# Optimization experiments

Measured on AMD Instinct MI355X. Metric: run time of the kernel, lower is better.

## Reference

```python
import jax, jax.numpy as jnp
import numpy as np

POOLING_COUNTS = [15, 8, 8]
N = 128
D = 256
B = 16


def _build_specs():
    # Replicates the (kernel, stride, i, j) schedule of SparseConv.__init__.
    specs = []
    stride, offset = 1, 0
    for ci, c in enumerate(POOLING_COUNTS):
        for k in range(c):
            offset += stride
            i = np.arange(0, N - offset, stride)
            j = np.arange(offset, N, stride)
            kern = 3 if (ci > 0 and k == 0) else 2  # first conv of later groups downsamples
            st = 2 if (ci > 0 and k == 0) else 1
            specs.append((kern, st, i, j))
        stride *= 2
    return specs

SPECS = _build_specs()
N_K2 = sum(1 for s in SPECS if s[0] == 2)  # 29 kernel-2 stride-1 convs
N_K3 = sum(1 for s in SPECS if s[0] == 3)  # 2 kernel-3 stride-2 convs


def _conv1d(x, w, b, stride):
    # x: (B, D, L), w: (O, I, K) -> (B, O, L_out), VALID padding like nn.Conv1d
    y = jax.lax.conv_general_dilated(x, w, (stride,), 'VALID',
                                     dimension_numbers=('NCH', 'OIH', 'NCH'))
    return y + b[None, :, None]


def setup_inputs() -> dict:
    key = jax.random.key(0)
    ks = jax.random.split(key, 5)
    scale = 1.0 / np.sqrt(2.0 * D)  # ~ PyTorch Conv1d default init scale
    return {
        'x': jax.random.normal(ks[0], (B, D, N), jnp.float32),
        'w2': jax.random.normal(ks[1], (N_K2, D, D, 2), jnp.float32) * scale,
        'b2': jax.random.normal(ks[2], (N_K2, D), jnp.float32) * scale,
        'w3': jax.random.normal(ks[3], (N_K3, D, D, 3), jnp.float32) * scale,
        'b3': jax.random.normal(ks[4], (N_K3, D), jnp.float32) * scale,
    }


def reference(x, w2, b2, w3, b3):
    diag = np.arange(N)
    # map2d[:, :, i, i] = x
    map2d = jnp.zeros((B, D, N, N), x.dtype).at[:, :, diag, diag].set(x)
    c2 = c3 = 0
    for kern, st, i, j in SPECS:  # fixed-length chain of 31 structurally distinct convs
        if kern == 2:
            x = _conv1d(x, w2[c2], b2[c2], 1)
            c2 += 1
        else:
            x = _conv1d(x, w3[c3], b3[c3], 2)
            c3 += 1
        map2d = map2d.at[:, :, i, j].set(x)  # scatter stripe into sparse 2D map
    return map2d
```

## Files before the change

kernel.cpp:

```cpp
#include <hip/hip_runtime.h>

typedef __bf16 bf16x8 __attribute__((ext_vector_type(8)));
typedef float  floatx4 __attribute__((ext_vector_type(4)));
typedef float  fvec4  __attribute__((ext_vector_type(4)));
typedef unsigned short ushort4v __attribute__((ext_vector_type(4)));
typedef unsigned short ushort8v __attribute__((ext_vector_type(8)));

__device__ __forceinline__ unsigned short f2bf(float f) {
  unsigned int u = __float_as_uint(f);
  u = u + 0x7FFFu + ((u >> 16) & 1u);
  return (unsigned short)(u >> 16);
}

#define WP3_OFF   3801088
#define X0_OFF    4194304
#define Y_OFF_B   (64u << 20)

__global__ __launch_bounds__(256) void prep_kernel(
    const float* __restrict__ w2, const float* __restrict__ w3,
    const float* __restrict__ x, unsigned short* __restrict__ ws)
{
  int g = blockIdx.x * 256 + threadIdx.x;
  const float* src; unsigned short* dst;
  if (g < 950272)            { src = w2; dst = ws; }
  else if (g < 950272+98304) { g -= 950272; src = w3; dst = ws + WP3_OFF; }
  else                       { g -= (950272+98304); src = x; dst = ws + X0_OFF; }
  fvec4 v = *reinterpret_cast<const fvec4*>(src + 4*g);
  ushort4v o;
  o[0] = f2bf(v[0]); o[1] = f2bf(v[1]); o[2] = f2bf(v[2]); o[3] = f2bf(v[3]);
  *reinterpret_cast<ushort4v*>(dst + 4*g) = o;
}

template<int KW>
__global__ __launch_bounds__(256) void conv_kernel(
    const unsigned short* __restrict__ Xin,
    unsigned short* __restrict__ Xout,
    const unsigned short* __restrict__ WP,
    const float* __restrict__ bias,
    float* __restrict__ Yl,
    int Lin, int Lpin, int Lout, int Lpout)
{
  constexpr int CS   = (KW == 3) ? 2 : 1;
  constexpr int KS   = 256 * KW;
  constexpr int pitch = KS + 8;
  constexpr int NV   = (KW == 2) ? 5 : 9;
  __shared__ unsigned short LA[32 * pitch];

  const int tid = threadIdx.x;
  const int b   = blockIdx.z;
  const int m0  = blockIdx.x * 32;
  const int n0  = blockIdx.y * 64;

  {
    const int i = tid;
    const unsigned short* rp = Xin + ((b * 256 + i) * Lpin) + CS * m0;
    ushort8v xr[NV];
#pragma unroll
    for (int v = 0; v < NV; ++v)
      xr[v] = *reinterpret_cast<const ushort8v*>(rp + v * 8);
    const unsigned short* xs = reinterpret_cast<const unsigned short*>(xr);
    if (KW == 2) {
#pragma unroll
      for (int m = 0; m < 32; ++m) {
        unsigned int pk = (unsigned int)xs[m] | ((unsigned int)xs[m + 1] << 16);
        *reinterpret_cast<unsigned int*>(&LA[m * pitch + 2 * i]) = pk;
      }
    } else {
#pragma unroll
      for (int m = 0; m < 32; ++m) {
        int base = m * pitch + 3 * i;
        LA[base]     = xs[2 * m];
        LA[base + 1] = xs[2 * m + 1];
        LA[base + 2] = xs[2 * m + 2];
      }
    }
  }
  __syncthreads();

  const int wave = tid >> 6, lane = tid & 63;
  const int l15 = lane & 15, quad = lane >> 4;
  const int nn = n0 + wave * 16 + l15;
  const unsigned short* wrow = WP + (long)nn * KS;
  const int kbase = quad * 8;

  floatx4 acc0 = {0.f, 0.f, 0.f, 0.f};
  floatx4 acc1 = {0.f, 0.f, 0.f, 0.f};

  constexpr int niter = KS / 32;
#pragma unroll
  for (int kc = 0; kc < niter; ++kc) {
    int ko = kc * 32 + kbase;
    bf16x8 bfrag = *reinterpret_cast<const bf16x8*>(wrow + ko);
    bf16x8 a0 = *reinterpret_cast<const bf16x8*>(&LA[l15 * pitch + ko]);
    bf16x8 a1 = *reinterpret_cast<const bf16x8*>(&LA[(16 + l15) * pitch + ko]);
    acc0 = __builtin_amdgcn_mfma_f32_16x16x32_bf16(a0, bfrag, acc0, 0, 0, 0);
    acc1 = __builtin_amdgcn_mfma_f32_16x16x32_bf16(a1, bfrag, acc1, 0, 0, 0);
  }

  const float bv = bias[nn];
  const int row = b * 256 + nn;
  unsigned short* xo = Xout + row * Lpout;
  float* yo = Yl + row * 128;
#pragma unroll
  for (int r = 0; r < 4; ++r) {
    int m = m0 + quad * 4 + r;
    if (m < Lout) {
      float v = acc0[r] + bv;
      xo[m] = f2bf(v);
      yo[m] = v;
    }
    int m2 = m0 + 16 + quad * 4 + r;
    if (m2 < Lout) {
      float v = acc1[r] + bv;
      xo[m2] = f2bf(v);
      yo[m2] = v;
    }
  }
}

__global__ __launch_bounds__(256) void assemble_kernel(
    float* __restrict__ out, const float* __restrict__ x, const float* __restrict__ Y)
{
  const int f0 = blockIdx.x * 256 + threadIdx.x;
  const int c4 = f0 & 31, r = (f0 >> 5) & 127;
  const int bch0 = f0 >> 12;

  int addr[4];
  bool dg[4];
#pragma unroll
  for (int jj = 0; jj < 4; ++jj) {
    int c = 4 * c4 + jj;
    int d = c - r;
    dg[jj] = (d == 0);
    int a = -1;
    if (d >= 1 && d <= 15) {
      a = (d - 1) * 524288 + r;
    } else if (d >= 17 && d <= 31 && (d & 1) == 1 && (r & 1) == 0) {
      a = (15 + ((d - 17) >> 1)) * 524288 + (r >> 1);
    } else if (d >= 35 && d <= 63 && (d & 3) == 3 && (r & 3) == 0) {
      a = (23 + ((d - 35) >> 2)) * 524288 + (r >> 2);
    }
    addr[jj] = a;
  }

  for (int it = 0; it < 32; ++it) {
    int bch = bch0 + it * 128;
    fvec4 v = {0.f, 0.f, 0.f, 0.f};
    int boff = bch * 128;
#pragma unroll
    for (int jj = 0; jj < 4; ++jj) {
      if (dg[jj])            v[jj] = x[boff + r];
      else if (addr[jj] >= 0) v[jj] = Y[addr[jj] + boff];
    }
    *reinterpret_cast<fvec4*>(out + (long)4 * (f0 + it * 524288)) = v;
  }
}

extern "C" void kernel_launch(void* const* d_in, const int* in_sizes, int n_in,
                              void* d_out, int out_size, void* d_ws, size_t ws_size,
                              hipStream_t stream)
{
  const float* x  = (const float*)d_in[0];
  const float* w2 = (const float*)d_in[1];
  const float* b2 = (const float*)d_in[2];
  const float* w3 = (const float*)d_in[3];
  const float* b3 = (const float*)d_in[4];
  float* out = (float*)d_out;
  unsigned short* ws = (unsigned short*)d_ws;
  float* Y = (float*)((char*)d_ws + Y_OFF_B);

  prep_kernel<<<4608, 256, 0, stream>>>(w2, w3, x, ws);

  const int counts[3] = {15, 8, 8};
  int stride = 1, offset = 0;
  int Lin = 128, Lpin = 128;
  int c2 = 0, c3 = 0, lidx = 0;
  long xprev = X0_OFF;
  long xnext = xprev + (long)16 * 256 * 128 + 64;
  for (int ci = 0; ci < 3; ++ci) {
    for (int k = 0; k < counts[ci]; ++k) {
      offset += stride;
      int KW = (ci > 0 && k == 0) ? 3 : 2;
      int cs = (KW == 3) ? 2 : 1;
      int Lout = (Lin - KW) / cs + 1;
      int Lpout = (Lout + 7) & ~7;
      const unsigned short* WPt; const float* bt;
      if (KW == 2) { WPt = ws + (long)c2 * 131072; bt = b2 + c2 * 256; ++c2; }
      else         { WPt = ws + WP3_OFF + (long)c3 * 196608; bt = b3 + c3 * 256; ++c3; }
      dim3 grid((Lout + 31) / 32, 4, 16);
      if (KW == 2)
        conv_kernel<2><<<grid, 256, 0, stream>>>(
            ws + xprev, ws + xnext, WPt, bt, Y + (long)lidx * 524288,
            Lin, Lpin, Lout, Lpout);
      else
        conv_kernel<3><<<grid, 256, 0, stream>>>(
            ws + xprev, ws + xnext, WPt, bt, Y + (long)lidx * 524288,
            Lin, Lpin, Lout, Lpout);
      ++lidx;
      xprev = xnext;
      xnext += (long)16 * 256 * Lpout + 64;
      Lin = Lout; Lpin = Lpout;
    }
    stride *= 2;
  }

  assemble_kernel<<<2048, 256, 0, stream>>>(out, x, Y);
}
```

Before: 585.5 us.

## Fuse all 31 conv layers into one persistent per-batch kernel with LDS-resident activations

Replaces 31 separate conv launches with a single chain kernel. It runs one 1024-thread block per batch element, and each block keeps the im2col-packed activation in shared memory across all layers. Each layer's epilogue writes its bf16 outputs straight into the next layer's packed LDS layout, so there are no global activation round-trips and no per-layer launch overhead. The cost is parallelism: only 16 workgroups on a large GPU, each streaming all the weights from L2/HBM, so throughput may be limited by low occupancy and serial weight reads.

```diff
diff --git a/kernel.cpp b/kernel.cpp
--- a/kernel.cpp
+++ b/kernel.cpp
@@ -4,7 +4,6 @@
 typedef float  floatx4 __attribute__((ext_vector_type(4)));
 typedef float  fvec4  __attribute__((ext_vector_type(4)));
 typedef unsigned short ushort4v __attribute__((ext_vector_type(4)));
-typedef unsigned short ushort8v __attribute__((ext_vector_type(8)));
 
 __device__ __forceinline__ unsigned short f2bf(float f) {
   unsigned int u = __float_as_uint(f);
@@ -13,109 +12,149 @@
 }
 
 #define WP3_OFF   3801088
-#define X0_OFF    4194304
 #define Y_OFF_B   (64u << 20)
 
 __global__ __launch_bounds__(256) void prep_kernel(
     const float* __restrict__ w2, const float* __restrict__ w3,
-    const float* __restrict__ x, unsigned short* __restrict__ ws)
+    unsigned short* __restrict__ ws)
 {
   int g = blockIdx.x * 256 + threadIdx.x;
   const float* src; unsigned short* dst;
-  if (g < 950272)            { src = w2; dst = ws; }
-  else if (g < 950272+98304) { g -= 950272; src = w3; dst = ws + WP3_OFF; }
-  else                       { g -= (950272+98304); src = x; dst = ws + X0_OFF; }
+  if (g < 950272) { src = w2; dst = ws; }
+  else            { g -= 950272; src = w3; dst = ws + WP3_OFF; }
   fvec4 v = *reinterpret_cast<const fvec4*>(src + 4*g);
   ushort4v o;
   o[0] = f2bf(v[0]); o[1] = f2bf(v[1]); o[2] = f2bf(v[2]); o[3] = f2bf(v[3]);
   *reinterpret_cast<ushort4v*>(dst + 4*g) = o;
 }
 
-template<int KW>
-__global__ __launch_bounds__(256) void conv_kernel(
-    const unsigned short* __restrict__ Xin,
-    unsigned short* __restrict__ Xout,
-    const unsigned short* __restrict__ WP,
-    const float* __restrict__ bias,
-    float* __restrict__ Yl,
-    int Lin, int Lpin, int Lout, int Lpout)
-{
-  constexpr int CS   = (KW == 3) ? 2 : 1;
-  constexpr int KS   = 256 * KW;
-  constexpr int pitch = KS + 8;
-  constexpr int NV   = (KW == 2) ? 5 : 9;
-  __shared__ unsigned short LA[32 * pitch];
-
-  const int tid = threadIdx.x;
-  const int b   = blockIdx.z;
-  const int m0  = blockIdx.x * 32;
-  const int n0  = blockIdx.y * 64;
-
-  {
-    const int i = tid;
-    const unsigned short* rp = Xin + ((b * 256 + i) * Lpin) + CS * m0;
-    ushort8v xr[NV];
-#pragma unroll
-    for (int v = 0; v < NV; ++v)
-      xr[v] = *reinterpret_cast<const ushort8v*>(rp + v * 8);
-    const unsigned short* xs = reinterpret_cast<const unsigned short*>(xr);
-    if (KW == 2) {
-#pragma unroll
-      for (int m = 0; m < 32; ++m) {
-        unsigned int pk = (unsigned int)xs[m] | ((unsigned int)xs[m + 1] << 16);
-        *reinterpret_cast<unsigned int*>(&LA[m * pitch + 2 * i]) = pk;
-      }
-    } else {
-#pragma unroll
-      for (int m = 0; m < 32; ++m) {
-        int base = m * pitch + 3 * i;
-        LA[base]     = xs[2 * m];
-        LA[base + 1] = xs[2 * m + 1];
-        LA[base + 2] = xs[2 * m + 2];
-      }
-    }
-  }
-  __syncthreads();
+
+template<int KW, int MTH, int KWN>
+__device__ __forceinline__ void step(
+    unsigned short* LA, int b, int Lout, int LoutN,
+    const unsigned short* __restrict__ W, const float* __restrict__ bias,
+    float* __restrict__ Yl, int tid)
+{
+  constexpr int K   = 256 * KW;
+  constexpr int P   = K + 8;
+  constexpr int NIT = K / 32;
+  constexpr int PN  = (KWN == 3) ? 776 : 520;
 
   const int wave = tid >> 6, lane = tid & 63;
   const int l15 = lane & 15, quad = lane >> 4;
-  const int nn = n0 + wave * 16 + l15;
-  const unsigned short* wrow = WP + (long)nn * KS;
-  const int kbase = quad * 8;
-
-  floatx4 acc0 = {0.f, 0.f, 0.f, 0.f};
-  floatx4 acc1 = {0.f, 0.f, 0.f, 0.f};
-
-  constexpr int niter = KS / 32;
-#pragma unroll
-  for (int kc = 0; kc < niter; ++kc) {
-    int ko = kc * 32 + kbase;
-    bf16x8 bfrag = *reinterpret_cast<const bf16x8*>(wrow + ko);
-    bf16x8 a0 = *reinterpret_cast<const bf16x8*>(&LA[l15 * pitch + ko]);
-    bf16x8 a1 = *reinterpret_cast<const bf16x8*>(&LA[(16 + l15) * pitch + ko]);
-    acc0 = __builtin_amdgcn_mfma_f32_16x16x32_bf16(a0, bfrag, acc0, 0, 0, 0);
-    acc1 = __builtin_amdgcn_mfma_f32_16x16x32_bf16(a1, bfrag, acc1, 0, 0, 0);
-  }
-
-  const float bv = bias[nn];
-  const int row = b * 256 + nn;
-  unsigned short* xo = Xout + row * Lpout;
-  float* yo = Yl + row * 128;
-#pragma unroll
-  for (int r = 0; r < 4; ++r) {
-    int m = m0 + quad * 4 + r;
-    if (m < Lout) {
-      float v = acc0[r] + bv;
-      xo[m] = f2bf(v);
-      yo[m] = v;
-    }
-    int m2 = m0 + 16 + quad * 4 + r;
-    if (m2 < Lout) {
-      float v = acc1[r] + bv;
-      xo[m2] = f2bf(v);
-      yo[m2] = v;
-    }
-  }
+  const int n0 = (wave >> 1) * 32;
+  const int mh = wave & 1;
+  const int nA = n0 + l15, nB = nA + 16;
+
+  const unsigned short* wAp = W + nA * K + quad * 8;
+  const unsigned short* wBp = W + nB * K + quad * 8;
+
+  floatx4 acc[2][MTH];
+#pragma unroll
+  for (int p = 0; p < 2; ++p)
+#pragma unroll
+    for (int t = 0; t < MTH; ++t) acc[p][t] = (floatx4){0.f, 0.f, 0.f, 0.f};
+
+  int aoff[MTH];
+#pragma unroll
+  for (int t = 0; t < MTH; ++t)
+    aoff[t] = ((mh * MTH + t) * 16 + l15) * P + quad * 8;
+
+#pragma unroll
+  for (int kc = 0; kc < NIT; ++kc) {
+    bf16x8 bA = *reinterpret_cast<const bf16x8*>(wAp + kc * 32);
+    bf16x8 bB = *reinterpret_cast<const bf16x8*>(wBp + kc * 32);
+#pragma unroll
+    for (int t = 0; t < MTH; ++t) {
+      bf16x8 a = *reinterpret_cast<const bf16x8*>(&LA[aoff[t] + kc * 32]);
+      acc[0][t] = __builtin_amdgcn_mfma_f32_16x16x32_bf16(a, bA, acc[0][t], 0, 0, 0);
+      acc[1][t] = __builtin_amdgcn_mfma_f32_16x16x32_bf16(a, bB, acc[1][t], 0, 0, 0);
+    }
+  }
+  __syncthreads();
+
+  const float bvA = bias[nA], bvB = bias[nB];
+#pragma unroll
+  for (int p = 0; p < 2; ++p) {
+    const int n = p ? nB : nA;
+    const float bv = p ? bvB : bvA;
+    float* yrow = Yl + (b * 256 + n) * 128;
+#pragma unroll
+    for (int t = 0; t < MTH; ++t) {
+      const int mbase = (mh * MTH + t) * 16 + quad * 4;
+      float vs[4];
+#pragma unroll
+      for (int r = 0; r < 4; ++r) {
+        const int m = mbase + r;
+        const float v = acc[p][t][r] + bv;
+        vs[r] = v;
+        if (m < Lout) {
+          const unsigned short bf = f2bf(v);
+          if (KWN == 2) {
+            if (m < LoutN) LA[m * PN + 2 * n]           = bf;
+            if (m >= 1)    LA[(m - 1) * PN + 2 * n + 1] = bf;
+          } else if (KWN == 3) {
+            if ((m & 1) == 0) {
+              if ((m >> 1) < LoutN) LA[(m >> 1) * PN + 3 * n]           = bf;
+              if (m >= 2)           LA[((m - 2) >> 1) * PN + 3 * n + 2] = bf;
+            } else {
+              if ((m >> 1) < LoutN) LA[(m >> 1) * PN + 3 * n + 1]       = bf;
+            }
+          }
+        }
+      }
+      if (mbase + 4 <= Lout) {
+        *reinterpret_cast<fvec4*>(yrow + mbase) = (fvec4){vs[0], vs[1], vs[2], vs[3]};
+      } else {
+#pragma unroll
+        for (int r = 0; r < 4; ++r)
+          if (mbase + r < Lout) yrow[mbase + r] = vs[r];
+      }
+    }
+  }
+  __syncthreads();
+}
+
+__global__ __launch_bounds__(1024) void chain_kernel(
+    const float* __restrict__ x, const float* __restrict__ b2,
+    const float* __restrict__ b3, const unsigned short* __restrict__ wsw,
+    float* __restrict__ Y)
+{
+  __shared__ unsigned short LA[66560];
+  const int b   = blockIdx.x;
+  const int tid = threadIdx.x;
+
+  for (int idx = tid; idx < 32768; idx += 1024) {
+    const int i = idx & 255, m = idx >> 8;
+    const unsigned short bf = f2bf(x[(b * 256 + i) * 128 + m]);
+    if (m < 127) LA[m * 520 + 2 * i]           = bf;
+    if (m >= 1)  LA[(m - 1) * 520 + 2 * i + 1] = bf;
+  }
+  __syncthreads();
+
+  const unsigned short* wp2 = wsw;
+  const unsigned short* wp3 = wsw + WP3_OFF;
+
+#pragma unroll 1
+  for (int l = 0; l < 14; ++l)
+    step<2, 4, 2>(LA, b, 127 - l, 126 - l, wp2 + l * 131072, b2 + l * 256,
+                  Y + (long)l * 524288, tid);
+  step<2, 4, 3>(LA, b, 113, 56, wp2 + 14 * 131072, b2 + 14 * 256,
+                Y + (long)14 * 524288, tid);
+  step<3, 2, 2>(LA, b, 56, 55, wp3, b3, Y + (long)15 * 524288, tid);
+#pragma unroll 1
+  for (int l = 16; l < 22; ++l)
+    step<2, 2, 2>(LA, b, 71 - l, 70 - l, wp2 + (l - 1) * 131072, b2 + (l - 1) * 256,
+                  Y + (long)l * 524288, tid);
+  step<2, 2, 3>(LA, b, 49, 24, wp2 + 21 * 131072, b2 + 21 * 256,
+                Y + (long)22 * 524288, tid);
+  step<3, 1, 2>(LA, b, 24, 23, wp3 + 196608, b3 + 256, Y + (long)23 * 524288, tid);
+#pragma unroll 1
+  for (int l = 24; l < 30; ++l)
+    step<2, 1, 2>(LA, b, 47 - l, 46 - l, wp2 + (l - 2) * 131072, b2 + (l - 2) * 256,
+                  Y + (long)l * 524288, tid);
+  step<2, 1, 0>(LA, b, 17, 0, wp2 + 28 * 131072, b2 + 28 * 256,
+                Y + (long)30 * 524288, tid);
 }
 
 __global__ __launch_bounds__(256) void assemble_kernel(
@@ -149,7 +188,7 @@
     int boff = bch * 128;
 #pragma unroll
     for (int jj = 0; jj < 4; ++jj) {
-      if (dg[jj])            v[jj] = x[boff + r];
+      if (dg[jj])             v[jj] = x[boff + r];
       else if (addr[jj] >= 0) v[jj] = Y[addr[jj] + boff];
     }
     *reinterpret_cast<fvec4*>(out + (long)4 * (f0 + it * 524288)) = v;
@@ -169,40 +208,7 @@
   unsigned short* ws = (unsigned short*)d_ws;
   float* Y = (float*)((char*)d_ws + Y_OFF_B);
 
-  prep_kernel<<<4608, 256, 0, stream>>>(w2, w3, x, ws);
-
-  const int counts[3] = {15, 8, 8};
-  int stride = 1, offset = 0;
-  int Lin = 128, Lpin = 128;
-  int c2 = 0, c3 = 0, lidx = 0;
-  long xprev = X0_OFF;
-  long xnext = xprev + (long)16 * 256 * 128 + 64;
-  for (int ci = 0; ci < 3; ++ci) {
-    for (int k = 0; k < counts[ci]; ++k) {
-      offset += stride;
-      int KW = (ci > 0 && k == 0) ? 3 : 2;
-      int cs = (KW == 3) ? 2 : 1;
-      int Lout = (Lin - KW) / cs + 1;
-      int Lpout = (Lout + 7) & ~7;
-      const unsigned short* WPt; const float* bt;
-      if (KW == 2) { WPt = ws + (long)c2 * 131072; bt = b2 + c2 * 256; ++c2; }
-      else         { WPt = ws + WP3_OFF + (long)c3 * 196608; bt = b3 + c3 * 256; ++c3; }
-      dim3 grid((Lout + 31) / 32, 4, 16);
-      if (KW == 2)
-        conv_kernel<2><<<grid, 256, 0, stream>>>(
-            ws + xprev, ws + xnext, WPt, bt, Y + (long)lidx * 524288,
-            Lin, Lpin, Lout, Lpout);
-      else
-        conv_kernel<3><<<grid, 256, 0, stream>>>(
-            ws + xprev, ws + xnext, WPt, bt, Y + (long)lidx * 524288,
-            Lin, Lpin, Lout, Lpout);
-      ++lidx;
-      xprev = xnext;
-      xnext += (long)16 * 256 * Lpout + 64;
-      Lin = Lout; Lpin = Lpout;
-    }
-    stride *= 2;
-  }
-
+  prep_kernel<<<4096, 256, 0, stream>>>(w2, w3, ws);
+  chain_kernel<<<16, 1024, 0, stream>>>(x, b2, b3, ws, Y);
   assemble_kernel<<<2048, 256, 0, stream>>>(out, x, Y);
 }
```

After: 888.3 us. 1.52x slower.

## Stage per-channel stripe values in shared memory for assemble kernel

Applied to the files above, without the earlier changes.

The assemble kernel now gives each block one (batch, channel) plane. It first loads all 31 conv-output stripes plus the diagonal input row into shared memory with coalesced reads, then writes the 128x128 output tile from LDS. Before, each thread gathered scattered Y values straight from global memory across 32 planes. This is meant to make the output-writing phase's reads coalesced and cached, at the cost of a block-wide sync and more blocks.

```diff
diff --git a/kernel.cpp b/kernel.cpp
--- a/kernel.cpp
+++ b/kernel.cpp
@@ -121,38 +121,45 @@
 __global__ __launch_bounds__(256) void assemble_kernel(
     float* __restrict__ out, const float* __restrict__ x, const float* __restrict__ Y)
 {
-  const int f0 = blockIdx.x * 256 + threadIdx.x;
-  const int c4 = f0 & 31, r = (f0 >> 5) & 127;
-  const int bch0 = f0 >> 12;
-
-  int addr[4];
-  bool dg[4];
-#pragma unroll
-  for (int jj = 0; jj < 4; ++jj) {
-    int c = 4 * c4 + jj;
-    int d = c - r;
-    dg[jj] = (d == 0);
-    int a = -1;
-    if (d >= 1 && d <= 15) {
-      a = (d - 1) * 524288 + r;
-    } else if (d >= 17 && d <= 31 && (d & 1) == 1 && (r & 1) == 0) {
-      a = (15 + ((d - 17) >> 1)) * 524288 + (r >> 1);
-    } else if (d >= 35 && d <= 63 && (d & 3) == 3 && (r & 3) == 0) {
-      a = (23 + ((d - 35) >> 2)) * 524288 + (r >> 2);
-    }
-    addr[jj] = a;
-  }
-
-  for (int it = 0; it < 32; ++it) {
-    int bch = bch0 + it * 128;
+  __shared__ float S[32 * 129];
+  const int blk = blockIdx.x;
+  const int tid = threadIdx.x;
+
+  {
+    const int m = tid & 127, half = tid >> 7;
+#pragma unroll
+    for (int lp = 0; lp < 16; ++lp) {
+      const int l = lp * 2 + half;
+      if (l < 31) {
+        const int Lout = (l < 15) ? (127 - l)
+                       : (l == 15) ? 56
+                       : (l < 23)  ? (71 - l)
+                       : (l == 23) ? 24 : (47 - l);
+        if (m < Lout) S[l * 129 + m] = Y[(long)l * 524288 + blk * 128 + m];
+      } else {
+        S[31 * 129 + m] = x[blk * 128 + m];
+      }
+    }
+  }
+  __syncthreads();
+
+  const long obase = (long)blk << 14;
+#pragma unroll 1
+  for (int it = 0; it < 16; ++it) {
+    const int flat = it * 256 + tid;
+    const int r = flat >> 5, c0 = (flat & 31) << 2;
     fvec4 v = {0.f, 0.f, 0.f, 0.f};
-    int boff = bch * 128;
 #pragma unroll
     for (int jj = 0; jj < 4; ++jj) {
-      if (dg[jj])            v[jj] = x[boff + r];
-      else if (addr[jj] >= 0) v[jj] = Y[addr[jj] + boff];
-    }
-    *reinterpret_cast<fvec4*>(out + (long)4 * (f0 + it * 524288)) = v;
+      const int d = c0 + jj - r;
+      if (d == 0)                 v[jj] = S[31 * 129 + r];
+      else if (d >= 1 && d <= 15) v[jj] = S[(d - 1) * 129 + r];
+      else if (d >= 17 && d <= 31 && (d & 1) == 1 && (r & 1) == 0)
+        v[jj] = S[(15 + ((d - 17) >> 1)) * 129 + (r >> 1)];
+      else if (d >= 35 && d <= 63 && (d & 3) == 3 && (r & 3) == 0)
+        v[jj] = S[(23 + ((d - 35) >> 2)) * 129 + (r >> 2)];
+    }
+    *reinterpret_cast<fvec4*>(out + obase + 4 * flat) = v;
   }
 }
 
@@ -204,5 +211,5 @@
     stride *= 2;
   }
 
-  assemble_kernel<<<2048, 256, 0, stream>>>(out, x, Y);
-}
+  assemble_kernel<<<4096, 256, 0, stream>>>(out, x, Y);
+}
```

Measured after the change: 540.8 us. -7.6%, faster.
